# Optimization experiments

Measured on AMD Instinct MI355X. Metric: run time of the kernel, lower is better.

## Reference

```python
import jax, jax.numpy as jnp
import numpy as np

N, IN_FEATS, OUT_FEATS = 8192, 512, 256


def setup_inputs() -> dict:
    key = jax.random.key(0)
    k1, k2, k3, k4 = jax.random.split(key, 4)
    feature_mat = jax.random.normal(k1, (N, IN_FEATS), dtype=jnp.float32)
    # Xavier-uniform style init for W and W2
    limW = float(np.sqrt(6.0 / (IN_FEATS + OUT_FEATS)))
    W = jax.random.uniform(k2, (IN_FEATS, OUT_FEATS), minval=-limW, maxval=limW, dtype=jnp.float32)
    limW2 = float(np.sqrt(6.0 / (2 * OUT_FEATS + 1)))
    W2 = jax.random.uniform(k3, (2 * OUT_FEATS, 1), minval=-limW2, maxval=limW2, dtype=jnp.float32)
    adj_mat = jax.random.randint(k4, (N, N), 0, 2, dtype=jnp.int32)
    return {"feature_mat": feature_mat, "W": W, "W2": W2, "adj_mat": adj_mat}


def reference(feature_mat, W, W2, adj_mat):
    out_feats = W.shape[1]
    Wh = feature_mat @ W                      # [N, F']
    Wh1 = Wh @ W2[:out_feats, :]              # [N, 1]
    Wh2 = Wh @ W2[out_feats:, :]              # [N, 1]
    e = Wh1 + Wh2.T                           # [N, N] broadcast add
    e = jnp.where(e > 0, e, 0.2 * e)          # leaky_relu(0.2)
    # NOTE: original masks with ZERO (not -inf) before softmax — faithful.
    e = jnp.where(adj_mat > 0, e, jnp.zeros((), dtype=e.dtype))
    attention = jax.nn.softmax(e, axis=1)     # row softmax over all N
    h_prime = attention @ Wh                  # [N, F']
    return jax.nn.relu(h_prime)
```

## Files before the change

### kernel.cpp

```cpp
#include <hip/hip_runtime.h>
#include <cstdint>
#include <cstddef>

#define NR 8192
#define FOUT 256
#define KIN 512
#define KSPLIT 4
#define JCHUNK (NR / KSPLIT)
#define BKJ 64
#define NSTEP (JCHUNK / BKJ)
#define IROWS 64

typedef __attribute__((ext_vector_type(8))) short bf16x8;
typedef __attribute__((ext_vector_type(4))) float f32x4;

__device__ __forceinline__ unsigned f2bf(float x) {
  unsigned u = __float_as_uint(x);
  u += 0x7fffu + ((u >> 16) & 1u);
  return u >> 16;
}
__device__ __forceinline__ float bf2f(unsigned h) {
  return __uint_as_float(h << 16);
}
__device__ __forceinline__ unsigned fkey(float x) {
  unsigned u = __float_as_uint(x);
  return (u & 0x80000000u) ? ~u : (u | 0x80000000u);
}
__device__ __forceinline__ float fkey_dec(unsigned k) {
  return __uint_as_float((k & 0x80000000u) ? (k ^ 0x80000000u) : ~k);
}

#define GLDS(g, l)                                                            \
  __builtin_amdgcn_global_load_lds(                                           \
      (const __attribute__((address_space(1))) unsigned int*)(g),             \
      (__attribute__((address_space(3))) unsigned int*)(l), 16, 0, 0)

__global__ __launch_bounds__(256) void k0_prep(const float* __restrict__ W,
                                               const float* __restrict__ W2,
                                               float* __restrict__ w1,
                                               float* __restrict__ w2,
                                               char* __restrict__ WTbf,
                                               unsigned* __restrict__ maxkey) {
  if (blockIdx.x == 0 && threadIdx.x == 0) *maxkey = 0u;
  int wv = threadIdx.x >> 6, lane = threadIdx.x & 63;
  int k = blockIdx.x * 4 + wv;
  int f4 = lane * 4;
  float4 wr = *(const float4*)(W + (size_t)k * FOUT + f4);
  float4 a = *(const float4*)(W2 + f4);
  float4 b = *(const float4*)(W2 + FOUT + f4);
  float d1 = wr.x * a.x + wr.y * a.y + wr.z * a.z + wr.w * a.w;
  float d2 = wr.x * b.x + wr.y * b.y + wr.z * b.z + wr.w * b.w;
#pragma unroll
  for (int off = 32; off; off >>= 1) {
    d1 += __shfl_xor(d1, off);
    d2 += __shfl_xor(d2, off);
  }
  if (lane == 0) {
    w1[k] = d1;
    w2[k] = d2;
  }
  int kt = k >> 5, kl = k & 31;
  float wv4[4] = {wr.x, wr.y, wr.z, wr.w};
#pragma unroll
  for (int ff = 0; ff < 4; ++ff) {
    int f = f4 + ff;
    size_t addr = (size_t)kt * 16384 + (f >> 4) * 1024 +
                  (((f & 15) | (((kl >> 3) & 3) << 4)) * 16) + (kl & 7) * 2;
    *(unsigned short*)(WTbf + addr) = (unsigned short)f2bf(wv4[ff]);
  }
}

__global__ __launch_bounds__(256) void k2_fused(
    const float* __restrict__ X, const char* __restrict__ WTbf,
    const float* __restrict__ w1, const float* __restrict__ w2,
    char* __restrict__ WhTf, float* __restrict__ Wh1, float* __restrict__ Wh2,
    unsigned* __restrict__ maxkey) {
  __shared__ char smem[2 * 18432 + 4096];
  char* buf0 = smem;
  char* buf1 = smem + 18432;
  char* wlds = smem + 2 * 18432;
  int t = threadIdx.x, wv = t >> 6, lane = t & 63;
  int jb = blockIdx.x * 32;
  int jr = t >> 3, koff = (t & 7) * 4;
  int cA = (jr & 15) | (((koff >> 3) & 3) << 4);
  int swA = cA ^ (((cA >> 4) & 3) << 2);
  int aoff = (jr >> 4) * 1024 + swA * 16 + ((koff & 4) << 1);
  int slotR = lane ^ (((lane >> 4) & 3) << 2);
  const float* xrow = X + (size_t)(jb + jr) * KIN + koff;

  {
    float2 a_ = *(const float2*)(w1 + t * 2);
    float2 b_ = *(const float2*)(w2 + t * 2);
    *(float2*)(wlds + t * 8) = a_;
    *(float2*)(wlds + 2048 + t * 8) = b_;
  }
  __syncthreads();

  float4 st0, st1, st2, st3;
  float d1 = 0.f, d2 = 0.f;
  f32x4 acc[2][4];
#pragma unroll
  for (int a = 0; a < 2; ++a)
#pragma unroll
    for (int b = 0; b < 4; ++b) acc[a][b] = (f32x4){0.f, 0.f, 0.f, 0.f};

#define K2_GLB(KT, BUFW)                                                      \
  do {                                                                        \
    const char* gs_ = WTbf + ((size_t)(KT) << 14) + (wv << 12) + lane * 16;   \
    char* ld_ = (BUFW) + 2048 + (wv << 12);                                   \
    GLDS(gs_, ld_);                                                           \
    GLDS(gs_ + 1024, ld_ + 1024);                                             \
    GLDS(gs_ + 2048, ld_ + 2048);                                             \
    GLDS(gs_ + 3072, ld_ + 3072);                                             \
  } while (0)

#define K2_LDX(KT, ST) (ST) = *(const float4*)(xrow + (KT) * 32)

#define K2_AGEN(ST, BUFW, SNUM)                                               \
  do {                                                                        \
    uint2 a_;                                                                 \
    a_.x = f2bf((ST).x) | (f2bf((ST).y) << 16);                               \
    a_.y = f2bf((ST).z) | (f2bf((ST).w) << 16);                               \
    *(uint2*)((BUFW) + aoff) = a_;                                            \
    float4 wa_ = *(const float4*)(wlds + ((SNUM)*32 + koff) * 4);             \
    float4 wb_ = *(const float4*)(wlds + 2048 + ((SNUM)*32 + koff) * 4);      \
    d1 += (ST).x * wa_.x + (ST).y * wa_.y + (ST).z * wa_.z + (ST).w * wa_.w;  \
    d2 += (ST).x * wb_.x + (ST).y * wb_.y + (ST).z * wb_.z + (ST).w * wb_.w;  \
  } while (0)

#define K2_ITER(S, BUFR, BUFW, STC, STF)                                      \
  do {                                                                        \
    int s_ = (S);                                                             \
    if (s_ + 1 < 16) K2_GLB(s_ + 1, BUFW);                                    \
    K2_LDX((s_ + 3 < 16) ? s_ + 3 : 15, STF);                                 \
    if (s_ + 1 < 16) K2_AGEN(STC, BUFW, s_ + 1);                              \
    bf16x8 a0 = *(const bf16x8*)((BUFR) + slotR * 16);                        \
    bf16x8 a1 = *(const bf16x8*)((BUFR) + 1024 + slotR * 16);                 \
    bf16x8 b0 = *(const bf16x8*)((BUFR) + 2048 + (wv * 4 + 0) * 1024 + lane * 16); \
    bf16x8 b1 = *(const bf16x8*)((BUFR) + 2048 + (wv * 4 + 1) * 1024 + lane * 16); \
    bf16x8 b2 = *(const bf16x8*)((BUFR) + 2048 + (wv * 4 + 2) * 1024 + lane * 16); \
    bf16x8 b3 = *(const bf16x8*)((BUFR) + 2048 + (wv * 4 + 3) * 1024 + lane * 16); \
    acc[0][0] = __builtin_amdgcn_mfma_f32_16x16x32_bf16(a0, b0, acc[0][0], 0, 0, 0); \
    acc[0][1] = __builtin_amdgcn_mfma_f32_16x16x32_bf16(a0, b1, acc[0][1], 0, 0, 0); \
    acc[0][2] = __builtin_amdgcn_mfma_f32_16x16x32_bf16(a0, b2, acc[0][2], 0, 0, 0); \
    acc[0][3] = __builtin_amdgcn_mfma_f32_16x16x32_bf16(a0, b3, acc[0][3], 0, 0, 0); \
    acc[1][0] = __builtin_amdgcn_mfma_f32_16x16x32_bf16(a1, b0, acc[1][0], 0, 0, 0); \
    acc[1][1] = __builtin_amdgcn_mfma_f32_16x16x32_bf16(a1, b1, acc[1][1], 0, 0, 0); \
    acc[1][2] = __builtin_amdgcn_mfma_f32_16x16x32_bf16(a1, b2, acc[1][2], 0, 0, 0); \
    acc[1][3] = __builtin_amdgcn_mfma_f32_16x16x32_bf16(a1, b3, acc[1][3], 0, 0, 0); \
    __builtin_amdgcn_sched_barrier(0);                                        \
    asm volatile("s_waitcnt vmcnt(1)");                                       \
    asm volatile("s_waitcnt lgkmcnt(0)");                                     \
    __builtin_amdgcn_s_barrier();                                             \
    __builtin_amdgcn_sched_barrier(0);                                        \
  } while (0)

  K2_GLB(0, buf0);
  K2_LDX(0, st0);
  K2_LDX(1, st1);
  K2_LDX(2, st2);
  K2_AGEN(st0, buf0, 0);
  __builtin_amdgcn_sched_barrier(0);
  asm volatile("s_waitcnt vmcnt(2)");
  asm volatile("s_waitcnt lgkmcnt(0)");
  __builtin_amdgcn_s_barrier();
  __builtin_amdgcn_sched_barrier(0);

  for (int s4 = 0; s4 < 16; s4 += 4) {
    K2_ITER(s4 + 0, buf0, buf1, st1, st3);
    K2_ITER(s4 + 1, buf1, buf0, st2, st0);
    K2_ITER(s4 + 2, buf0, buf1, st3, st1);
    K2_ITER(s4 + 3, buf1, buf0, st0, st2);
  }
#undef K2_ITER
#undef K2_AGEN
#undef K2_LDX
#undef K2_GLB

  int q = lane >> 4;
#pragma unroll
  for (int mi = 0; mi < 2; ++mi)
#pragma unroll
    for (int nn = 0; nn < 4; ++nn) {
      int u2 = wv * 4 + nn;
      int cell = (lane & 15) | ((((mi * 2) + (q >> 1)) & 3) << 4);
      uint2 v;
      v.x = f2bf(acc[mi][nn].x) | (f2bf(acc[mi][nn].y) << 16);
      v.y = f2bf(acc[mi][nn].z) | (f2bf(acc[mi][nn].w) << 16);
      *(uint2*)(buf0 + 2048 + u2 * 1024 + cell * 16 + ((q & 1) << 3)) = v;
    }
  __syncthreads();
  char* wb = WhTf + (size_t)blockIdx.x * 16384;
#pragma unroll
  for (int q2 = 0; q2 < 4; ++q2) {
    uint4 v = *(const uint4*)(buf0 + 2048 + q2 * 4096 + t * 16);
    *(uint4*)(wb + q2 * 4096 + t * 16) = v;
  }

  d1 += __shfl_xor(d1, 1);
  d1 += __shfl_xor(d1, 2);
  d1 += __shfl_xor(d1, 4);
  d2 += __shfl_xor(d2, 1);
  d2 += __shfl_xor(d2, 2);
  d2 += __shfl_xor(d2, 4);
  if ((t & 7) == 0) {
    Wh1[jb + jr] = d1;
    Wh2[jb + jr] = d2;
  }
  float mx = d2;
#pragma unroll
  for (int off = 32; off >= 8; off >>= 1) mx = fmaxf(mx, __shfl_xor(mx, off));
  __shared__ float red[4];
  if (lane == 0) red[wv] = mx;
  __syncthreads();
  if (t == 0) {
    float bm = fmaxf(fmaxf(red[0], red[1]), fmaxf(red[2], red[3]));
    atomicMax(maxkey, fkey(bm));
  }
}

__device__ __forceinline__ uint2 hv4(int4 aq, float4 wq, float wh1, float m,
                                     float enm, float& z) {
  float s0 = wh1 + wq.x, s1 = wh1 + wq.y, s2 = wh1 + wq.z, s3 = wh1 + wq.w;
  s0 = s0 > 0.f ? s0 : 0.2f * s0;
  s1 = s1 > 0.f ? s1 : 0.2f * s1;
  s2 = s2 > 0.f ? s2 : 0.2f * s2;
  s3 = s3 > 0.f ? s3 : 0.2f * s3;
  float w0 = aq.x > 0 ? __expf(s0 - m) : enm;
  float w1 = aq.y > 0 ? __expf(s1 - m) : enm;
  float w2 = aq.z > 0 ? __expf(s2 - m) : enm;
  float w3 = aq.w > 0 ? __expf(s3 - m) : enm;
  unsigned h0 = f2bf(w0), h1 = f2bf(w1), h2 = f2bf(w2), h3 = f2bf(w3);
  z += bf2f(h0) + bf2f(h1) + bf2f(h2) + bf2f(h3);
  uint2 r;
  r.x = h0 | (h1 << 16);
  r.y = h2 | (h3 << 16);
  return r;
}
__device__ __forceinline__ uint4 hv8(int4 a0, int4 a1, float4 w0, float4 w1,
                                     float wh1, float m, float enm, float& z) {
  uint2 r0 = hv4(a0, w0, wh1, m, enm, z);
  uint2 r1 = hv4(a1, w1, wh1, m, enm, z);
  return (uint4){r0.x, r0.y, r1.x, r1.y};
}

__global__ __launch_bounds__(512, 4) void k3_attn(
    const int* __restrict__ adj, const char* __restrict__ WhTf,
    const float* __restrict__ Wh1, const float* __restrict__ Wh2,
    const unsigned* __restrict__ maxptr, float* __restrict__ PVp,
    float* __restrict__ Zp) {
  __shared__ char smem[24576];
  char* abuf0 = smem;
  char* abuf1 = smem + 8192;
  char* wlds = smem + 16384;
  int t = threadIdx.x, wv = t >> 6, lane = t & 63;
  int kc = blockIdx.x & 3;
  int ib = blockIdx.x >> 2;
  int ibase = ib * IROWS;
  int jbch = kc * JCHUNK;
  int r0 = t >> 3;
  int j8 = (t & 7) * 8;
  int iglob = ibase + r0;
  float maxwh2 = fkey_dec(*maxptr);
  float wh1 = Wh1[iglob];
  float m = fmaxf(0.f, wh1 + maxwh2);
  float enm = __expf(-m);
  int unitA = (r0 >> 4) * 2 + (j8 >> 5);
  int cA = (r0 & 15) | (((j8 & 31) >> 3) << 4);
  int swA = cA ^ (((cA >> 4) & 3) << 2);
  int aoff = unitA * 1024 + swA * 16;
  int slotR = lane ^ (((lane >> 4) & 3) << 2);
  const int* adjrow = adj + ((size_t)iglob << 13) + jbch + j8;
  const char* bbase = WhTf + ((size_t)(kc * 64) << 14) +
                      (size_t)(wv * 2) * 1024 + (size_t)lane * 16;
  const char* wl = wlds + j8 * 4;

  *(float4*)(wlds + t * 16) = *(const float4*)(Wh2 + jbch + t * 4);
  __syncthreads();

  bf16x8 bA0, bA1, bA2, bA3, bB0, bB1, bB2, bB3;
  int4 st0_a, st0_b, st1_a, st1_b;
  f32x4 acc[4][2];
#pragma unroll
  for (int a = 0; a < 4; ++a)
#pragma unroll
    for (int b = 0; b < 2; ++b) acc[a][b] = (f32x4){0.f, 0.f, 0.f, 0.f};
  float zacc = 0.f;

#define K3_LDB(S, B0, B1, B2, B3)                                             \
  do {                                                                        \
    int sc_ = (S) < NSTEP ? (S) : NSTEP - 1;                                  \
    const char* bp_ = bbase + (size_t)(2 * sc_) * 16384;                      \
    B0 = *(const bf16x8*)(bp_);                                               \
    B1 = *(const bf16x8*)(bp_ + 1024);                                        \
    B2 = *(const bf16x8*)(bp_ + 16384);                                       \
    B3 = *(const bf16x8*)(bp_ + 16384 + 1024);                                \
  } while (0)

#define K3_LDA(S, ST)                                                         \
  do {                                                                        \
    int sc_ = (S) < NSTEP ? (S) : NSTEP - 1;                                  \
    ST##_a = *(const int4*)(adjrow + sc_ * BKJ);                              \
    ST##_b = *(const int4*)(adjrow + sc_ * BKJ + 4);                          \
  } while (0)

#define K3_ITER(S, AR, AW, BC0, BC1, BC2, BC3, BF0, BF1, BF2, BF3, STC, DO_HV) \
  do {                                                                        \
    int s_ = (S);                                                             \
    K3_LDB(s_ + 1, BF0, BF1, BF2, BF3);                                       \
    if (DO_HV) {                                                              \
      float4 wq0_ = *(const float4*)(wl + (s_ + 1) * 256);                    \
      float4 wq1_ = *(const float4*)(wl + (s_ + 1) * 256 + 16);               \
      uint4 a_ = hv8(STC##_a, STC##_b, wq0_, wq1_, wh1, m, enm, zacc);        \
      *(uint4*)((AW) + aoff) = a_;                                            \
    }                                                                         \
    K3_LDA(s_ + 3, STC);                                                      \
    _Pragma("unroll")                                                         \
    for (int rf_ = 0; rf_ < 4; ++rf_) {                                       \
      bf16x8 ak0_ = *(const bf16x8*)((AR) + (rf_ * 2 + 0) * 1024 + slotR * 16); \
      bf16x8 ak1_ = *(const bf16x8*)((AR) + (rf_ * 2 + 1) * 1024 + slotR * 16); \
      acc[rf_][0] = __builtin_amdgcn_mfma_f32_16x16x32_bf16(ak0_, BC0, acc[rf_][0], 0, 0, 0); \
      acc[rf_][1] = __builtin_amdgcn_mfma_f32_16x16x32_bf16(ak0_, BC1, acc[rf_][1], 0, 0, 0); \
      acc[rf_][0] = __builtin_amdgcn_mfma_f32_16x16x32_bf16(ak1_, BC2, acc[rf_][0], 0, 0, 0); \
      acc[rf_][1] = __builtin_amdgcn_mfma_f32_16x16x32_bf16(ak1_, BC3, acc[rf_][1], 0, 0, 0); \
    }                                                                         \
    __builtin_amdgcn_sched_barrier(0);                                        \
    asm volatile("s_waitcnt lgkmcnt(0)" ::: "memory");                        \
    __builtin_amdgcn_s_barrier();                                             \
    __builtin_amdgcn_sched_barrier(0);                                        \
  } while (0)

  K3_LDB(0, bA0, bA1, bA2, bA3);
  int4 adj0a = *(const int4*)(adjrow);
  int4 adj0b = *(const int4*)(adjrow + 4);
  K3_LDA(1, st1);
  K3_LDA(2, st0);
  {
    float4 wq0 = *(const float4*)(wl);
    float4 wq1 = *(const float4*)(wl + 16);
    uint4 a0 = hv8(adj0a, adj0b, wq0, wq1, wh1, m, enm, zacc);
    *(uint4*)(abuf0 + aoff) = a0;
  }
  __builtin_amdgcn_sched_barrier(0);
  asm volatile("s_waitcnt lgkmcnt(0)" ::: "memory");
  __builtin_amdgcn_s_barrier();
  __builtin_amdgcn_sched_barrier(0);

  for (int s2 = 0; s2 < NSTEP - 2; s2 += 2) {
    K3_ITER(s2 + 0, abuf0, abuf1, bA0, bA1, bA2, bA3, bB0, bB1, bB2, bB3, st1, 1);
    K3_ITER(s2 + 1, abuf1, abuf0, bB0, bB1, bB2, bB3, bA0, bA1, bA2, bA3, st0, 1);
  }
  K3_ITER(NSTEP - 2, abuf0, abuf1, bA0, bA1, bA2, bA3, bB0, bB1, bB2, bB3, st1, 1);
  K3_ITER(NSTEP - 1, abuf1, abuf0, bB0, bB1, bB2, bB3, bA0, bA1, bA2, bA3, st0, 0);
#undef K3_ITER
#undef K3_LDA
#undef K3_LDB

  zacc += __shfl_xor(zacc, 1);
  zacc += __shfl_xor(zacc, 2);
  zacc += __shfl_xor(zacc, 4);
  if ((t & 7) == 0) Zp[(size_t)kc * NR + iglob] = zacc;
#pragma unroll
  for (int rf = 0; rf < 4; ++rf)
#pragma unroll
    for (int un = 0; un < 2; ++un) {
      int f = (wv * 2 + un) * 16 + (lane & 15);
      int row0 = ibase + rf * 16 + ((lane >> 4) << 2);
      size_t base = ((size_t)kc * NR + row0) * FOUT + f;
      PVp[base + 0 * FOUT] = acc[rf][un].x;
      PVp[base + 1 * FOUT] = acc[rf][un].y;
      PVp[base + 2 * FOUT] = acc[rf][un].z;
      PVp[base + 3 * FOUT] = acc[rf][un].w;
    }
}

__global__ __launch_bounds__(256) void k4_reduce(const float* __restrict__ PVp,
                                                 const float* __restrict__ Zp,
                                                 float* __restrict__ out) {
  int tid = blockIdx.x * 256 + threadIdx.x;
  int i = tid >> 6;
  int f4 = (tid & 63) * 4;
  float z = Zp[i] + Zp[NR + i] + Zp[2 * NR + i] + Zp[3 * NR + i];
  float4 a = {0.f, 0.f, 0.f, 0.f};
#pragma unroll
  for (int c = 0; c < KSPLIT; ++c) {
    float4 p = *(const float4*)(PVp + ((size_t)c * NR + i) * FOUT + f4);
    a.x += p.x;
    a.y += p.y;
    a.z += p.z;
    a.w += p.w;
  }
  float inv = 1.f / z;
  float4 r;
  r.x = fmaxf(a.x * inv, 0.f);
  r.y = fmaxf(a.y * inv, 0.f);
  r.z = fmaxf(a.z * inv, 0.f);
  r.w = fmaxf(a.w * inv, 0.f);
  *(float4*)(out + (size_t)i * FOUT + f4) = r;
}

extern "C" void kernel_launch(void* const* d_in, const int* in_sizes, int n_in,
                              void* d_out, int out_size, void* d_ws,
                              size_t ws_size, hipStream_t stream) {
  const float* X = (const float*)d_in[0];
  const float* W = (const float*)d_in[1];
  const float* W2 = (const float*)d_in[2];
  const int* adj = (const int*)d_in[3];
  float* out = (float*)d_out;
  char* ws = (char*)d_ws;

  const size_t WHT_OFF = 0;
  const size_t WTBF_OFF = (size_t)4 * 1024 * 1024;
  const size_t W1_OFF = WTBF_OFF + 256 * 1024;
  const size_t W2V_OFF = W1_OFF + 2048;
  const size_t WH1_OFF = W2V_OFF + 2048;
  const size_t WH2_OFF = WH1_OFF + 32768;
  const size_t MXK_OFF = WH2_OFF + 32768;
  const size_t ZP_OFF = MXK_OFF + 256;
  const size_t PV_OFF = ZP_OFF + (size_t)KSPLIT * NR * 4;

  char* WhTf = ws + WHT_OFF;
  char* WTbf = ws + WTBF_OFF;
  float* w1 = (float*)(ws + W1_OFF);
  float* w2 = (float*)(ws + W2V_OFF);
  float* Wh1 = (float*)(ws + WH1_OFF);
  float* Wh2 = (float*)(ws + WH2_OFF);
  unsigned* maxkey = (unsigned*)(ws + MXK_OFF);
  float* Zp = (float*)(ws + ZP_OFF);
  float* PVp = (float*)(ws + PV_OFF);

  k0_prep<<<128, 256, 0, stream>>>(W, W2, w1, w2, WTbf, maxkey);
  k2_fused<<<256, 256, 0, stream>>>(X, WTbf, w1, w2, WhTf, Wh1, Wh2, maxkey);
  k3_attn<<<512, 512, 0, stream>>>(adj, WhTf, Wh1, Wh2, maxkey, PVp, Zp);
  k4_reduce<<<2048, 256, 0, stream>>>(PVp, Zp, out);
}
```

Measured before the change: 118.3 us.

## Double attention tile rows to 128 with 1024-thread blocks, one N-tile per wave

The attention kernel now processes 128 query rows per block with 16 waves, each owning a single 16-column slice of the output features, instead of 64 rows with 8 waves owning two slices each. Each Wh^T B-fragment is therefore reused across twice as many rows, halving global reads of Wh per row and halving the grid size. In exchange the blocks are larger, LDS use grows to 40 KB, and there are only 256 blocks, which may limit occupancy and make the barriers more expensive.

```diff
diff --git a/kernel.cpp b/kernel.cpp
--- a/kernel.cpp
+++ b/kernel.cpp
@@ -9,7 +9,7 @@
 #define JCHUNK (NR / KSPLIT)
 #define BKJ 64
 #define NSTEP (JCHUNK / BKJ)
-#define IROWS 64
+#define IROWS 128
 
 typedef __attribute__((ext_vector_type(8))) short bf16x8;
 typedef __attribute__((ext_vector_type(4))) float f32x4;
@@ -244,15 +244,15 @@
   return (uint4){r0.x, r0.y, r1.x, r1.y};
 }
 
-__global__ __launch_bounds__(512, 4) void k3_attn(
+__global__ __launch_bounds__(1024, 4) void k3_attn(
     const int* __restrict__ adj, const char* __restrict__ WhTf,
     const float* __restrict__ Wh1, const float* __restrict__ Wh2,
     const unsigned* __restrict__ maxptr, float* __restrict__ PVp,
     float* __restrict__ Zp) {
-  __shared__ char smem[24576];
+  __shared__ char smem[40960];
   char* abuf0 = smem;
-  char* abuf1 = smem + 8192;
-  char* wlds = smem + 16384;
+  char* abuf1 = smem + 16384;
+  char* wlds = smem + 32768;
   int t = threadIdx.x, wv = t >> 6, lane = t & 63;
   int kc = blockIdx.x & 3;
   int ib = blockIdx.x >> 2;
@@ -271,30 +271,26 @@
   int aoff = unitA * 1024 + swA * 16;
   int slotR = lane ^ (((lane >> 4) & 3) << 2);
   const int* adjrow = adj + ((size_t)iglob << 13) + jbch + j8;
-  const char* bbase = WhTf + ((size_t)(kc * 64) << 14) +
-                      (size_t)(wv * 2) * 1024 + (size_t)lane * 16;
+  const char* bbase = WhTf + ((size_t)(kc * 64) << 14) + (size_t)wv * 1024 +
+                      (size_t)lane * 16;
   const char* wl = wlds + j8 * 4;
 
-  *(float4*)(wlds + t * 16) = *(const float4*)(Wh2 + jbch + t * 4);
+  *(float2*)(wlds + t * 8) = *(const float2*)(Wh2 + jbch + t * 2);
   __syncthreads();
 
-  bf16x8 bA0, bA1, bA2, bA3, bB0, bB1, bB2, bB3;
+  bf16x8 bA0, bA1, bB0, bB1;
   int4 st0_a, st0_b, st1_a, st1_b;
-  f32x4 acc[4][2];
-#pragma unroll
-  for (int a = 0; a < 4; ++a)
-#pragma unroll
-    for (int b = 0; b < 2; ++b) acc[a][b] = (f32x4){0.f, 0.f, 0.f, 0.f};
+  f32x4 acc[8];
+#pragma unroll
+  for (int a = 0; a < 8; ++a) acc[a] = (f32x4){0.f, 0.f, 0.f, 0.f};
   float zacc = 0.f;
 
-#define K3_LDB(S, B0, B1, B2, B3)                                             \
+#define K3_LDB(S, B0, B1)                                                     \
   do {                                                                        \
     int sc_ = (S) < NSTEP ? (S) : NSTEP - 1;                                  \
     const char* bp_ = bbase + (size_t)(2 * sc_) * 16384;                      \
     B0 = *(const bf16x8*)(bp_);                                               \
-    B1 = *(const bf16x8*)(bp_ + 1024);                                        \
-    B2 = *(const bf16x8*)(bp_ + 16384);                                       \
-    B3 = *(const bf16x8*)(bp_ + 16384 + 1024);                                \
+    B1 = *(const bf16x8*)(bp_ + 16384);                                       \
   } while (0)
 
 #define K3_LDA(S, ST)                                                         \
@@ -304,10 +300,10 @@
     ST##_b = *(const int4*)(adjrow + sc_ * BKJ + 4);                          \
   } while (0)
 
-#define K3_ITER(S, AR, AW, BC0, BC1, BC2, BC3, BF0, BF1, BF2, BF3, STC, DO_HV) \
+#define K3_ITER(S, AR, AW, BC0, BC1, BF0, BF1, STC, DO_HV)                    \
   do {                                                                        \
     int s_ = (S);                                                             \
-    K3_LDB(s_ + 1, BF0, BF1, BF2, BF3);                                       \
+    K3_LDB(s_ + 1, BF0, BF1);                                                 \
     if (DO_HV) {                                                              \
       float4 wq0_ = *(const float4*)(wl + (s_ + 1) * 256);                    \
       float4 wq1_ = *(const float4*)(wl + (s_ + 1) * 256 + 16);               \
@@ -316,13 +312,11 @@
     }                                                                         \
     K3_LDA(s_ + 3, STC);                                                      \
     _Pragma("unroll")                                                         \
-    for (int rf_ = 0; rf_ < 4; ++rf_) {                                       \
+    for (int rf_ = 0; rf_ < 8; ++rf_) {                                       \
       bf16x8 ak0_ = *(const bf16x8*)((AR) + (rf_ * 2 + 0) * 1024 + slotR * 16); \
       bf16x8 ak1_ = *(const bf16x8*)((AR) + (rf_ * 2 + 1) * 1024 + slotR * 16); \
-      acc[rf_][0] = __builtin_amdgcn_mfma_f32_16x16x32_bf16(ak0_, BC0, acc[rf_][0], 0, 0, 0); \
-      acc[rf_][1] = __builtin_amdgcn_mfma_f32_16x16x32_bf16(ak0_, BC1, acc[rf_][1], 0, 0, 0); \
-      acc[rf_][0] = __builtin_amdgcn_mfma_f32_16x16x32_bf16(ak1_, BC2, acc[rf_][0], 0, 0, 0); \
-      acc[rf_][1] = __builtin_amdgcn_mfma_f32_16x16x32_bf16(ak1_, BC3, acc[rf_][1], 0, 0, 0); \
+      acc[rf_] = __builtin_amdgcn_mfma_f32_16x16x32_bf16(ak0_, BC0, acc[rf_], 0, 0, 0); \
+      acc[rf_] = __builtin_amdgcn_mfma_f32_16x16x32_bf16(ak1_, BC1, acc[rf_], 0, 0, 0); \
     }                                                                         \
     __builtin_amdgcn_sched_barrier(0);                                        \
     asm volatile("s_waitcnt lgkmcnt(0)" ::: "memory");                        \
@@ -330,7 +324,7 @@
     __builtin_amdgcn_sched_barrier(0);                                        \
   } while (0)
 
-  K3_LDB(0, bA0, bA1, bA2, bA3);
+  K3_LDB(0, bA0, bA1);
   int4 adj0a = *(const int4*)(adjrow);
   int4 adj0b = *(const int4*)(adjrow + 4);
   K3_LDA(1, st1);
@@ -347,11 +341,11 @@
   __builtin_amdgcn_sched_barrier(0);
 
   for (int s2 = 0; s2 < NSTEP - 2; s2 += 2) {
-    K3_ITER(s2 + 0, abuf0, abuf1, bA0, bA1, bA2, bA3, bB0, bB1, bB2, bB3, st1, 1);
-    K3_ITER(s2 + 1, abuf1, abuf0, bB0, bB1, bB2, bB3, bA0, bA1, bA2, bA3, st0, 1);
-  }
-  K3_ITER(NSTEP - 2, abuf0, abuf1, bA0, bA1, bA2, bA3, bB0, bB1, bB2, bB3, st1, 1);
-  K3_ITER(NSTEP - 1, abuf1, abuf0, bB0, bB1, bB2, bB3, bA0, bA1, bA2, bA3, st0, 0);
+    K3_ITER(s2 + 0, abuf0, abuf1, bA0, bA1, bB0, bB1, st1, 1);
+    K3_ITER(s2 + 1, abuf1, abuf0, bB0, bB1, bA0, bA1, st0, 1);
+  }
+  K3_ITER(NSTEP - 2, abuf0, abuf1, bA0, bA1, bB0, bB1, st1, 1);
+  K3_ITER(NSTEP - 1, abuf1, abuf0, bB0, bB1, bA0, bA1, st0, 0);
 #undef K3_ITER
 #undef K3_LDA
 #undef K3_LDB
@@ -361,17 +355,15 @@
   zacc += __shfl_xor(zacc, 4);
   if ((t & 7) == 0) Zp[(size_t)kc * NR + iglob] = zacc;
 #pragma unroll
-  for (int rf = 0; rf < 4; ++rf)
-#pragma unroll
-    for (int un = 0; un < 2; ++un) {
-      int f = (wv * 2 + un) * 16 + (lane & 15);
-      int row0 = ibase + rf * 16 + ((lane >> 4) << 2);
-      size_t base = ((size_t)kc * NR + row0) * FOUT + f;
-      PVp[base + 0 * FOUT] = acc[rf][un].x;
-      PVp[base + 1 * FOUT] = acc[rf][un].y;
-      PVp[base + 2 * FOUT] = acc[rf][un].z;
-      PVp[base + 3 * FOUT] = acc[rf][un].w;
-    }
+  for (int rf = 0; rf < 8; ++rf) {
+    int f = wv * 16 + (lane & 15);
+    int row0 = ibase + rf * 16 + ((lane >> 4) << 2);
+    size_t base = ((size_t)kc * NR + row0) * FOUT + f;
+    PVp[base + 0 * FOUT] = acc[rf].x;
+    PVp[base + 1 * FOUT] = acc[rf].y;
+    PVp[base + 2 * FOUT] = acc[rf].z;
+    PVp[base + 3 * FOUT] = acc[rf].w;
+  }
 }
 
 __global__ __launch_bounds__(256) void k4_reduce(const float* __restrict__ PVp,
@@ -431,6 +423,6 @@
 
   k0_prep<<<128, 256, 0, stream>>>(W, W2, w1, w2, WTbf, maxkey);
   k2_fused<<<256, 256, 0, stream>>>(X, WTbf, w1, w2, WhTf, Wh1, Wh2, maxkey);
-  k3_attn<<<512, 512, 0, stream>>>(adj, WhTf, Wh1, Wh2, maxkey, PVp, Zp);
+  k3_attn<<<256, 1024, 0, stream>>>(adj, WhTf, Wh1, Wh2, maxkey, PVp, Zp);
   k4_reduce<<<2048, 256, 0, stream>>>(PVp, Zp, out);
 }
```

After: 113.0 us. 1.05x faster.

## Halve split-K in attention kernel and remap adjacency tiles to MFMA layout

Applied to the files above, without the earlier changes.

Split-K over the neighbour dimension drops from 4 to 2, so the attention kernel launches 256 blocks that each walk twice as many j-steps. This halves the partial PV and Z writes and the reads in the final reduce. The thread-to-adjacency mapping changes so each wave builds one 16-row by 32-column MFMA fragment directly. The adjacency prefetch deepens to four stages, and the row-sum Z is reduced through shared memory. The cost is fewer blocks (256 on 256 CUs, one each), longer serial loops, more registers and LDS, and a fmax-based leaky relu.

```diff
diff --git a/kernel.cpp b/kernel.cpp
--- a/kernel.cpp
+++ b/kernel.cpp
@@ -5,7 +5,7 @@
 #define NR 8192
 #define FOUT 256
 #define KIN 512
-#define KSPLIT 4
+#define KSPLIT 2
 #define JCHUNK (NR / KSPLIT)
 #define BKJ 64
 #define NSTEP (JCHUNK / BKJ)
@@ -222,10 +222,10 @@
 __device__ __forceinline__ uint2 hv4(int4 aq, float4 wq, float wh1, float m,
                                      float enm, float& z) {
   float s0 = wh1 + wq.x, s1 = wh1 + wq.y, s2 = wh1 + wq.z, s3 = wh1 + wq.w;
-  s0 = s0 > 0.f ? s0 : 0.2f * s0;
-  s1 = s1 > 0.f ? s1 : 0.2f * s1;
-  s2 = s2 > 0.f ? s2 : 0.2f * s2;
-  s3 = s3 > 0.f ? s3 : 0.2f * s3;
+  s0 = fmaxf(s0, 0.2f * s0);
+  s1 = fmaxf(s1, 0.2f * s1);
+  s2 = fmaxf(s2, 0.2f * s2);
+  s3 = fmaxf(s3, 0.2f * s3);
   float w0 = aq.x > 0 ? __expf(s0 - m) : enm;
   float w1 = aq.y > 0 ? __expf(s1 - m) : enm;
   float w2 = aq.z > 0 ? __expf(s2 - m) : enm;
@@ -244,42 +244,42 @@
   return (uint4){r0.x, r0.y, r1.x, r1.y};
 }
 
-__global__ __launch_bounds__(512, 4) void k3_attn(
+__global__ __launch_bounds__(512, 2) void k3_attn(
     const int* __restrict__ adj, const char* __restrict__ WhTf,
     const float* __restrict__ Wh1, const float* __restrict__ Wh2,
     const unsigned* __restrict__ maxptr, float* __restrict__ PVp,
     float* __restrict__ Zp) {
-  __shared__ char smem[24576];
+  __shared__ char smem[33280];
   char* abuf0 = smem;
   char* abuf1 = smem + 8192;
   char* wlds = smem + 16384;
+  float* zlds = (float*)(smem + 32768);
   int t = threadIdx.x, wv = t >> 6, lane = t & 63;
-  int kc = blockIdx.x & 3;
-  int ib = blockIdx.x >> 2;
+  int kc = blockIdx.x & 1;
+  int ib = blockIdx.x >> 1;
   int ibase = ib * IROWS;
   int jbch = kc * JCHUNK;
-  int r0 = t >> 3;
-  int j8 = (t & 7) * 8;
-  int iglob = ibase + r0;
+  int rg = wv >> 1, ks = wv & 1;
+  int genrow = ibase + rg * 16 + (lane & 15);
   float maxwh2 = fkey_dec(*maxptr);
-  float wh1 = Wh1[iglob];
+  float wh1 = Wh1[genrow];
   float m = fmaxf(0.f, wh1 + maxwh2);
   float enm = __expf(-m);
-  int unitA = (r0 >> 4) * 2 + (j8 >> 5);
-  int cA = (r0 & 15) | (((j8 & 31) >> 3) << 4);
-  int swA = cA ^ (((cA >> 4) & 3) << 2);
-  int aoff = unitA * 1024 + swA * 16;
-  int slotR = lane ^ (((lane >> 4) & 3) << 2);
-  const int* adjrow = adj + ((size_t)iglob << 13) + jbch + j8;
-  const char* bbase = WhTf + ((size_t)(kc * 64) << 14) +
+  int swA = lane ^ (((lane >> 4) & 3) << 2);
+  int aoff = (rg * 2 + ks) * 1024 + swA * 16;
+  int slotR = swA;
+  const int* adjrow = adj + ((size_t)genrow << 13) + jbch + ks * 32 +
+                      ((lane >> 4) << 3);
+  const char* bbase = WhTf + ((size_t)(kc * 128) << 14) +
                       (size_t)(wv * 2) * 1024 + (size_t)lane * 16;
-  const char* wl = wlds + j8 * 4;
-
-  *(float4*)(wlds + t * 16) = *(const float4*)(Wh2 + jbch + t * 4);
+  const char* wl = wlds + ks * 128 + ((lane >> 4) << 5);
+
+  *(float4*)(wlds + t * 32) = *(const float4*)(Wh2 + jbch + t * 8);
+  *(float4*)(wlds + t * 32 + 16) = *(const float4*)(Wh2 + jbch + t * 8 + 4);
   __syncthreads();
 
   bf16x8 bA0, bA1, bA2, bA3, bB0, bB1, bB2, bB3;
-  int4 st0_a, st0_b, st1_a, st1_b;
+  int4 st0_a, st0_b, st1_a, st1_b, st2_a, st2_b, st3_a, st3_b;
   f32x4 acc[4][2];
 #pragma unroll
   for (int a = 0; a < 4; ++a)
@@ -287,24 +287,24 @@
     for (int b = 0; b < 2; ++b) acc[a][b] = (f32x4){0.f, 0.f, 0.f, 0.f};
   float zacc = 0.f;
 
+#define K3_LDA(S, ST)                                                         \
+  do {                                                                        \
+    int sc_ = (S) < NSTEP ? (S) : NSTEP - 1;                                  \
+    ST##_a = *(const int4*)(adjrow + sc_ * 64);                               \
+    ST##_b = *(const int4*)(adjrow + sc_ * 64 + 4);                           \
+  } while (0)
+
 #define K3_LDB(S, B0, B1, B2, B3)                                             \
   do {                                                                        \
     int sc_ = (S) < NSTEP ? (S) : NSTEP - 1;                                  \
-    const char* bp_ = bbase + (size_t)(2 * sc_) * 16384;                      \
-    B0 = *(const bf16x8*)(bp_);                                               \
-    B1 = *(const bf16x8*)(bp_ + 1024);                                        \
-    B2 = *(const bf16x8*)(bp_ + 16384);                                       \
-    B3 = *(const bf16x8*)(bp_ + 16384 + 1024);                                \
-  } while (0)
-
-#define K3_LDA(S, ST)                                                         \
-  do {                                                                        \
-    int sc_ = (S) < NSTEP ? (S) : NSTEP - 1;                                  \
-    ST##_a = *(const int4*)(adjrow + sc_ * BKJ);                              \
-    ST##_b = *(const int4*)(adjrow + sc_ * BKJ + 4);                          \
-  } while (0)
-
-#define K3_ITER(S, AR, AW, BC0, BC1, BC2, BC3, BF0, BF1, BF2, BF3, STC, DO_HV) \
+    const char* bp_ = bbase + (size_t)(sc_ * 2) * 16384;                      \
+    B0 = *(const bf16x8*)(bp_);                                   \
+    B1 = *(const bf16x8*)(bp_ + 16384);                           \
+    B2 = *(const bf16x8*)(bp_ + 1024);                            \
+    B3 = *(const bf16x8*)(bp_ + 16384 + 1024);                    \
+  } while (0)
+
+#define K3_ITER(S, AR, AW, STC, BC0, BC1, BC2, BC3, BF0, BF1, BF2, BF3, DO_HV) \
   do {                                                                        \
     int s_ = (S);                                                             \
     K3_LDB(s_ + 1, BF0, BF1, BF2, BF3);                                       \
@@ -314,15 +314,15 @@
       uint4 a_ = hv8(STC##_a, STC##_b, wq0_, wq1_, wh1, m, enm, zacc);        \
       *(uint4*)((AW) + aoff) = a_;                                            \
     }                                                                         \
-    K3_LDA(s_ + 3, STC);                                                      \
+    K3_LDA(s_ + 5, STC);                                                      \
     _Pragma("unroll")                                                         \
     for (int rf_ = 0; rf_ < 4; ++rf_) {                                       \
-      bf16x8 ak0_ = *(const bf16x8*)((AR) + (rf_ * 2 + 0) * 1024 + slotR * 16); \
-      bf16x8 ak1_ = *(const bf16x8*)((AR) + (rf_ * 2 + 1) * 1024 + slotR * 16); \
-      acc[rf_][0] = __builtin_amdgcn_mfma_f32_16x16x32_bf16(ak0_, BC0, acc[rf_][0], 0, 0, 0); \
-      acc[rf_][1] = __builtin_amdgcn_mfma_f32_16x16x32_bf16(ak0_, BC1, acc[rf_][1], 0, 0, 0); \
-      acc[rf_][0] = __builtin_amdgcn_mfma_f32_16x16x32_bf16(ak1_, BC2, acc[rf_][0], 0, 0, 0); \
-      acc[rf_][1] = __builtin_amdgcn_mfma_f32_16x16x32_bf16(ak1_, BC3, acc[rf_][1], 0, 0, 0); \
+      bf16x8 a0_ = *(const bf16x8*)((AR) + (rf_ * 2 + 0) * 1024 + slotR * 16); \
+      bf16x8 a1_ = *(const bf16x8*)((AR) + (rf_ * 2 + 1) * 1024 + slotR * 16); \
+      acc[rf_][0] = __builtin_amdgcn_mfma_f32_16x16x32_bf16(a0_, BC0, acc[rf_][0], 0, 0, 0); \
+      acc[rf_][1] = __builtin_amdgcn_mfma_f32_16x16x32_bf16(a0_, BC2, acc[rf_][1], 0, 0, 0); \
+      acc[rf_][0] = __builtin_amdgcn_mfma_f32_16x16x32_bf16(a1_, BC1, acc[rf_][0], 0, 0, 0); \
+      acc[rf_][1] = __builtin_amdgcn_mfma_f32_16x16x32_bf16(a1_, BC3, acc[rf_][1], 0, 0, 0); \
     }                                                                         \
     __builtin_amdgcn_sched_barrier(0);                                        \
     asm volatile("s_waitcnt lgkmcnt(0)" ::: "memory");                        \
@@ -331,14 +331,16 @@
   } while (0)
 
   K3_LDB(0, bA0, bA1, bA2, bA3);
-  int4 adj0a = *(const int4*)(adjrow);
-  int4 adj0b = *(const int4*)(adjrow + 4);
+  int4 adj0_a = *(const int4*)(adjrow);
+  int4 adj0_b = *(const int4*)(adjrow + 4);
   K3_LDA(1, st1);
-  K3_LDA(2, st0);
+  K3_LDA(2, st2);
+  K3_LDA(3, st3);
+  K3_LDA(4, st0);
   {
     float4 wq0 = *(const float4*)(wl);
     float4 wq1 = *(const float4*)(wl + 16);
-    uint4 a0 = hv8(adj0a, adj0b, wq0, wq1, wh1, m, enm, zacc);
+    uint4 a0 = hv8(adj0_a, adj0_b, wq0, wq1, wh1, m, enm, zacc);
     *(uint4*)(abuf0 + aoff) = a0;
   }
   __builtin_amdgcn_sched_barrier(0);
@@ -346,25 +348,34 @@
   __builtin_amdgcn_s_barrier();
   __builtin_amdgcn_sched_barrier(0);
 
-  for (int s2 = 0; s2 < NSTEP - 2; s2 += 2) {
-    K3_ITER(s2 + 0, abuf0, abuf1, bA0, bA1, bA2, bA3, bB0, bB1, bB2, bB3, st1, 1);
-    K3_ITER(s2 + 1, abuf1, abuf0, bB0, bB1, bB2, bB3, bA0, bA1, bA2, bA3, st0, 1);
-  }
-  K3_ITER(NSTEP - 2, abuf0, abuf1, bA0, bA1, bA2, bA3, bB0, bB1, bB2, bB3, st1, 1);
-  K3_ITER(NSTEP - 1, abuf1, abuf0, bB0, bB1, bB2, bB3, bA0, bA1, bA2, bA3, st0, 0);
+  for (int s4 = 0; s4 < NSTEP - 4; s4 += 4) {
+    K3_ITER(s4 + 0, abuf0, abuf1, st1, bA0, bA1, bA2, bA3, bB0, bB1, bB2, bB3, 1);
+    K3_ITER(s4 + 1, abuf1, abuf0, st2, bB0, bB1, bB2, bB3, bA0, bA1, bA2, bA3, 1);
+    K3_ITER(s4 + 2, abuf0, abuf1, st3, bA0, bA1, bA2, bA3, bB0, bB1, bB2, bB3, 1);
+    K3_ITER(s4 + 3, abuf1, abuf0, st0, bB0, bB1, bB2, bB3, bA0, bA1, bA2, bA3, 1);
+  }
+  K3_ITER(NSTEP - 4, abuf0, abuf1, st1, bA0, bA1, bA2, bA3, bB0, bB1, bB2, bB3, 1);
+  K3_ITER(NSTEP - 3, abuf1, abuf0, st2, bB0, bB1, bB2, bB3, bA0, bA1, bA2, bA3, 1);
+  K3_ITER(NSTEP - 2, abuf0, abuf1, st3, bA0, bA1, bA2, bA3, bB0, bB1, bB2, bB3, 1);
+  K3_ITER(NSTEP - 1, abuf1, abuf0, st0, bB0, bB1, bB2, bB3, bA0, bA1, bA2, bA3, 0);
 #undef K3_ITER
+#undef K3_LDB
 #undef K3_LDA
-#undef K3_LDB
-
-  zacc += __shfl_xor(zacc, 1);
-  zacc += __shfl_xor(zacc, 2);
-  zacc += __shfl_xor(zacc, 4);
-  if ((t & 7) == 0) Zp[(size_t)kc * NR + iglob] = zacc;
+
+  zacc += __shfl_xor(zacc, 16);
+  zacc += __shfl_xor(zacc, 32);
+  if (lane < 16) zlds[rg * 32 + ks * 16 + lane] = zacc;
+  __syncthreads();
+  if (t < IROWS) {
+    int rg2 = t >> 4, r2 = t & 15;
+    Zp[(size_t)kc * NR + ibase + t] =
+        zlds[rg2 * 32 + r2] + zlds[rg2 * 32 + 16 + r2];
+  }
 #pragma unroll
   for (int rf = 0; rf < 4; ++rf)
 #pragma unroll
     for (int un = 0; un < 2; ++un) {
-      int f = (wv * 2 + un) * 16 + (lane & 15);
+      int f = wv * 32 + un * 16 + (lane & 15);
       int row0 = ibase + rf * 16 + ((lane >> 4) << 2);
       size_t base = ((size_t)kc * NR + row0) * FOUT + f;
       PVp[base + 0 * FOUT] = acc[rf][un].x;
@@ -380,22 +391,15 @@
   int tid = blockIdx.x * 256 + threadIdx.x;
   int i = tid >> 6;
   int f4 = (tid & 63) * 4;
-  float z = Zp[i] + Zp[NR + i] + Zp[2 * NR + i] + Zp[3 * NR + i];
-  float4 a = {0.f, 0.f, 0.f, 0.f};
-#pragma unroll
-  for (int c = 0; c < KSPLIT; ++c) {
-    float4 p = *(const float4*)(PVp + ((size_t)c * NR + i) * FOUT + f4);
-    a.x += p.x;
-    a.y += p.y;
-    a.z += p.z;
-    a.w += p.w;
-  }
+  float z = Zp[i] + Zp[NR + i];
+  float4 p0 = *(const float4*)(PVp + (size_t)i * FOUT + f4);
+  float4 p1 = *(const float4*)(PVp + ((size_t)NR + i) * FOUT + f4);
   float inv = 1.f / z;
   float4 r;
-  r.x = fmaxf(a.x * inv, 0.f);
-  r.y = fmaxf(a.y * inv, 0.f);
-  r.z = fmaxf(a.z * inv, 0.f);
-  r.w = fmaxf(a.w * inv, 0.f);
+  r.x = fmaxf((p0.x + p1.x) * inv, 0.f);
+  r.y = fmaxf((p0.y + p1.y) * inv, 0.f);
+  r.z = fmaxf((p0.z + p1.z) * inv, 0.f);
+  r.w = fmaxf((p0.w + p1.w) * inv, 0.f);
   *(float4*)(out + (size_t)i * FOUT + f4) = r;
 }
 
@@ -431,6 +435,6 @@
 
   k0_prep<<<128, 256, 0, stream>>>(W, W2, w1, w2, WTbf, maxkey);
   k2_fused<<<256, 256, 0, stream>>>(X, WTbf, w1, w2, WhTf, Wh1, Wh2, maxkey);
-  k3_attn<<<512, 512, 0, stream>>>(adj, WhTf, Wh1, Wh2, maxkey, PVp, Zp);
+  k3_attn<<<256, 512, 0, stream>>>(adj, WhTf, Wh1, Wh2, maxkey, PVp, Zp);
   k4_reduce<<<2048, 256, 0, stream>>>(PVp, Zp, out);
 }
```

New measurement: 135.7 us. 1.15x slower.
